# Kernel optimization log

Hardware: AMD Instinct MI355X
Metric: run time of the kernel (lower is better)

## Reference

```python
import jax, jax.numpy as jnp
import numpy as np

N_NODES = 50000
N_EDGES = 800000
D_IN = 64      # in_node_features == in_edge_features
D_OUT = 64     # out_features


def _xavier(key, shape, gain):
    fan_in, fan_out = shape[1], shape[0]
    bound = gain * np.sqrt(6.0 / (fan_in + fan_out))
    return jax.random.uniform(key, shape, jnp.float32, -bound, bound)


def setup_inputs() -> dict:
    key = jax.random.key(0)
    ks = jax.random.split(key, 8)
    gain = np.sqrt(2.0)  # calculate_gain('relu')
    features = jax.random.normal(ks[0], (N_NODES, D_IN), jnp.float32)
    edge_index = jax.random.randint(ks[1], (2, N_EDGES), 0, N_NODES, jnp.int64)
    edge_features = jax.random.normal(ks[2], (N_EDGES, D_IN), jnp.float32)
    W1 = _xavier(ks[3], (D_OUT, 2 * D_IN + D_IN), gain)
    b1 = jnp.zeros((D_OUT,), jnp.float32)
    W2 = _xavier(ks[4], (D_IN, D_OUT), gain)
    b2 = jnp.zeros((D_IN,), jnp.float32)
    W3 = _xavier(ks[5], (D_OUT, 2 * D_IN), gain)
    b3 = jnp.zeros((D_OUT,), jnp.float32)
    W4 = _xavier(ks[6], (D_OUT, D_OUT), gain)  # W4 not xavier-reset in source but default init; xavier is fine for a numeric baseline
    b4 = jnp.zeros((D_OUT,), jnp.float32)
    return dict(features=features, edge_index=edge_index, edge_features=edge_features,
                W1=W1, b1=b1, W2=W2, b2=b2, W3=W3, b3=b3, W4=W4, b4=b4)


def reference(features, edge_index, edge_features, W1, b1, W2, b2, W3, b3, W4, b4):
    src, dst = edge_index[0], edge_index[1]
    # gather + concat: [E, 2*D_IN + D_IN]
    h_neigh = jnp.concatenate([features[src], edge_features, features[dst]], axis=-1)
    h_neigh = jax.nn.relu(h_neigh @ W1.T + b1)
    h_neigh = h_neigh @ W2.T + b2                       # [E, D_IN]
    # scatter-sum into a copy of features (out=h.clone(), reduce='sum')
    s = features + jax.ops.segment_sum(h_neigh, src, num_segments=features.shape[0])
    z = jax.nn.relu(jnp.concatenate([features, s], axis=-1) @ W3.T + b3)
    z = z @ W4.T + b4
    return z
```

## Files before the change

### kernel.cpp

```cpp
#include <hip/hip_runtime.h>

typedef __bf16 bf16;
typedef __bf16 bf16x4 __attribute__((ext_vector_type(4)));
typedef __bf16 bf16x8 __attribute__((ext_vector_type(8)));
typedef float  f32x4  __attribute__((ext_vector_type(4)));

#define MFMA16(a, b, c) __builtin_amdgcn_mfma_f32_16x16x32_bf16((a), (b), (c), 0, 0, 0)

constexpr int N_NODES = 50000;
constexpr int N_EDGES = 800000;
constexpr int D = 64;

constexpr size_t OFF_FBUF   = 0;
constexpr size_t OFF_H2     = 6400000;
constexpr size_t OFF_IPOS   = 108800000;
constexpr size_t OFF_ROWPTR = 112000000;
constexpr size_t OFF_CURSOR = 112200064;
constexpr size_t OFF_COUNTS = 112400064;
constexpr size_t OFF_WBF    = 112600064;
constexpr size_t OFF_FLAGS  = 112657408;
constexpr size_t WS_FAST_NEED = 112700000;

constexpr size_t S_SBUF  = 0;
constexpr size_t S_FLAGS = 12800000;

constexpr int XS_STRIDE = 200;
constexpr int HS_STRIDE = 72;
constexpr int X2_STRIDE = 136;
constexpr int W1_STRIDE = 200;
constexpr int W2_STRIDE = 72;
constexpr int W3_STRIDE = 136;
constexpr int W4_STRIDE = 72;

__global__ void detect_kernel(const void* __restrict__ feat,
                              const void* __restrict__ eidx,
                              int* __restrict__ flags)
{
    __shared__ int c_bf[64], c_nz[64];
    const int t = threadIdx.x;
    const unsigned short* h = (const unsigned short*)feat;
    int c = 0;
    #pragma unroll
    for (int j = 0; j < 8; ++j) {
        const unsigned short v = h[(t * 8 + j) * 2];
        const int e8 = (v >> 7) & 0xFF;
        c += (e8 >= 97 && e8 <= 157) ? 1 : 0;
    }
    c_bf[t] = c;
    const int* ei = (const int*)eidx;
    int nz = 0;
    #pragma unroll
    for (int j = 0; j < 2; ++j)
        nz += (ei[(t * 2 + j) * 2 + 1] != 0) ? 1 : 0;
    c_nz[t] = nz;
    __syncthreads();
    if (t == 0) {
        int s = 0, s2 = 0;
        for (int i = 0; i < 64; ++i) { s += c_bf[i]; s2 += c_nz[i]; }
        flags[0] = (s < 384) ? 1 : 0;
        flags[1] = (s2 < 4) ? 1 : 0;
    }
}

__device__ inline bf16x8 ld8(const void* base, size_t off, int f32f) {
    if (f32f) {
        const float* p = (const float*)base + off;
        const float4 a = *(const float4*)p;
        const float4 b = *(const float4*)(p + 4);
        bf16x8 r;
        r[0] = (bf16)a.x; r[1] = (bf16)a.y; r[2] = (bf16)a.z; r[3] = (bf16)a.w;
        r[4] = (bf16)b.x; r[5] = (bf16)b.y; r[6] = (bf16)b.z; r[7] = (bf16)b.w;
        return r;
    }
    return *(const bf16x8*)((const bf16*)base + off);
}

__device__ inline float ldf(const void* base, int i, int f32f) {
    return f32f ? ((const float*)base)[i] : (float)((const bf16*)base)[i];
}

__device__ inline int gidx(const void* e, size_t i, int i64f) {
    return i64f ? (int)((const long long*)e)[i] : ((const int*)e)[i];
}

__global__ void prep_kernel(const void* __restrict__ W1, const void* __restrict__ W2,
                            const void* __restrict__ W3, const void* __restrict__ W4,
                            bf16* __restrict__ wbf, const int* __restrict__ flags)
{
    const int F32 = flags[0];
    for (int i = threadIdx.x; i < 28672; i += 256) {
        const void* src; int off;
        if (i < 12288)      { src = W1; off = i; }
        else if (i < 16384) { src = W2; off = i - 12288; }
        else if (i < 24576) { src = W3; off = i - 16384; }
        else                { src = W4; off = i - 24576; }
        wbf[i] = F32 ? (bf16)((const float*)src)[off] : ((const bf16*)src)[off];
    }
}

__global__ void conv_feat_kernel(const void* __restrict__ feat, bf16* __restrict__ fbuf,
                                 const int* __restrict__ flags)
{
    const int F32 = flags[0];
    const int i = blockIdx.x * 256 + threadIdx.x;
    if (F32) {
        const float4 v = ((const float4*)feat)[i];
        bf16x4 r; r[0] = (bf16)v.x; r[1] = (bf16)v.y; r[2] = (bf16)v.z; r[3] = (bf16)v.w;
        ((bf16x4*)fbuf)[i] = r;
    } else {
        ((bf16x4*)fbuf)[i] = ((const bf16x4*)feat)[i];
    }
}

__global__ void hist_kernel(const void* __restrict__ eidx, int* __restrict__ counts,
                            const int* __restrict__ flags)
{
    const int I64 = flags[1];
    const int e = blockIdx.x * 256 + threadIdx.x;
    atomicAdd(&counts[gidx(eidx, e, I64)], 1);
}

__global__ void scan_kernel(const int* __restrict__ counts, int* __restrict__ rowptr,
                            int* __restrict__ cursor)
{
    __shared__ int part[256];
    const int t = threadIdx.x;
    const int base = t * 196;
    int s = 0;
    for (int g = 0; g < 49; ++g) {
        const int idx = base + g * 4;
        if (idx < N_NODES) {
            const int4 v = *(const int4*)&counts[idx];
            s += v.x + v.y + v.z + v.w;
        }
    }
    part[t] = s;
    __syncthreads();
    if (t == 0) {
        int acc = 0;
        for (int i = 0; i < 256; ++i) { const int v = part[i]; part[i] = acc; acc += v; }
        rowptr[N_NODES] = acc;
    }
    __syncthreads();
    int acc = part[t];
    for (int g = 0; g < 49; ++g) {
        const int idx = base + g * 4;
        if (idx < N_NODES) {
            const int4 v = *(const int4*)&counts[idx];
            int4 r;
            r.x = acc;
            r.y = acc + v.x;
            r.z = acc + v.x + v.y;
            r.w = acc + v.x + v.y + v.z;
            acc += v.x + v.y + v.z + v.w;
            *(int4*)&rowptr[idx] = r;
            *(int4*)&cursor[idx] = r;
        }
    }
}

__global__ void fill_kernel(const void* __restrict__ eidx, int* __restrict__ cursor,
                            int* __restrict__ ipos, const int* __restrict__ flags)
{
    const int I64 = flags[1];
    const int e = blockIdx.x * 256 + threadIdx.x;
    const int src = gidx(eidx, e, I64);
    ipos[e] = atomicAdd(&cursor[src], 1);
}

__global__ __launch_bounds__(256, 3) void edge_fast(
    const bf16* __restrict__ fbuf, const void* __restrict__ eidx,
    const void* __restrict__ efeat,
    const bf16* __restrict__ wbf, const void* __restrict__ b1, const void* __restrict__ b2,
    const int* __restrict__ ipos, bf16* __restrict__ h2ws, const int* __restrict__ flags)
{
    __shared__ bf16 W1l[64 * W1_STRIDE];
    __shared__ bf16 W2l[64 * W2_STRIDE];
    __shared__ bf16 hs[4][32 * 72];

    const int t    = threadIdx.x;
    const int wave = t >> 6;
    const int lane = t & 63;
    const int lrow = lane & 15;
    const int quad = lane >> 4;
    const int e0   = blockIdx.x * 128 + wave * 32;
    const int F32  = flags[0], I64 = flags[1];

    #pragma unroll
    for (int it = 0; it < 6; ++it) {
        const int idx = it * 256 + t;
        const int row = idx / 24;
        const int col = (idx - row * 24) * 8;
        *(bf16x8*)&W1l[row * W1_STRIDE + col] = *(const bf16x8*)&wbf[row * 192 + col];
    }
    #pragma unroll
    for (int it = 0; it < 2; ++it) {
        const int idx = it * 256 + t;
        const int row = idx >> 3;
        const int col = (idx & 7) * 8;
        *(bf16x8*)&W2l[row * W2_STRIDE + col] = *(const bf16x8*)&wbf[12288 + row * 64 + col];
    }
    __syncthreads();

    const int eA   = e0 + lrow;
    const int eB   = e0 + 16 + lrow;
    const int srcA = gidx(eidx, (size_t)eA, I64);
    const int dstA = gidx(eidx, (size_t)N_EDGES + eA, I64);
    const int srcB = gidx(eidx, (size_t)eB, I64);
    const int dstB = gidx(eidx, (size_t)N_EDGES + eB, I64);

    f32x4 acc[2][4] = {
        {{0,0,0,0},{0,0,0,0},{0,0,0,0},{0,0,0,0}},
        {{0,0,0,0},{0,0,0,0},{0,0,0,0},{0,0,0,0}}
    };
    #pragma unroll
    for (int k = 0; k < 6; ++k) {
        const int po = (k & 1) * 32 + quad * 8;
        bf16x8 a0, a1;
        if (k < 2) {
            a0 = *(const bf16x8*)&fbuf[(size_t)srcA * D + po];
            a1 = *(const bf16x8*)&fbuf[(size_t)srcB * D + po];
        } else if (k < 4) {
            a0 = ld8(efeat, (size_t)eA * D + po, F32);
            a1 = ld8(efeat, (size_t)eB * D + po, F32);
        } else {
            a0 = *(const bf16x8*)&fbuf[(size_t)dstA * D + po];
            a1 = *(const bf16x8*)&fbuf[(size_t)dstB * D + po];
        }
        #pragma unroll
        for (int n = 0; n < 4; ++n) {
            const bf16x8 b = *(const bf16x8*)&W1l[(n * 16 + lrow) * W1_STRIDE + k * 32 + quad * 8];
            acc[0][n] = MFMA16(a0, b, acc[0][n]);
            acc[1][n] = MFMA16(a1, b, acc[1][n]);
        }
    }

    #pragma unroll
    for (int n = 0; n < 4; ++n) {
        const int col  = n * 16 + lrow;
        const float bb = ldf(b1, col, F32);
        #pragma unroll
        for (int m = 0; m < 2; ++m) {
            #pragma unroll
            for (int r = 0; r < 4; ++r) {
                float v = acc[m][n][r] + bb;
                v = v > 0.f ? v : 0.f;
                hs[wave][(m * 16 + quad * 4 + r) * 72 + col] = (bf16)v;
            }
        }
    }

    f32x4 acc2[2][4] = {
        {{0,0,0,0},{0,0,0,0},{0,0,0,0},{0,0,0,0}},
        {{0,0,0,0},{0,0,0,0},{0,0,0,0},{0,0,0,0}}
    };
    #pragma unroll
    for (int k = 0; k < 2; ++k) {
        const bf16x8 a0 = *(const bf16x8*)&hs[wave][lrow * 72 + k * 32 + quad * 8];
        const bf16x8 a1 = *(const bf16x8*)&hs[wave][(16 + lrow) * 72 + k * 32 + quad * 8];
        #pragma unroll
        for (int n = 0; n < 4; ++n) {
            const bf16x8 b = *(const bf16x8*)&W2l[(n * 16 + lrow) * W2_STRIDE + k * 32 + quad * 8];
            acc2[0][n] = MFMA16(a0, b, acc2[0][n]);
            acc2[1][n] = MFMA16(a1, b, acc2[1][n]);
        }
    }

    #pragma unroll
    for (int n = 0; n < 4; ++n) {
        const int col  = n * 16 + lrow;
        const float bb = ldf(b2, col, F32);
        #pragma unroll
        for (int m = 0; m < 2; ++m) {
            #pragma unroll
            for (int r = 0; r < 4; ++r)
                hs[wave][(m * 16 + quad * 4 + r) * 72 + col] = (bf16)(acc2[m][n][r] + bb);
        }
    }

    const int row = lane >> 2;
    const int seg = lane & 3;
    #pragma unroll
    for (int m = 0; m < 2; ++m) {
        const int ip  = ipos[e0 + m * 16 + row];
        const bf16x8 v0 = *(const bf16x8*)&hs[wave][(m * 16 + row) * 72 + seg * 16];
        const bf16x8 v1 = *(const bf16x8*)&hs[wave][(m * 16 + row) * 72 + seg * 16 + 8];
        *(bf16x8*)&h2ws[(size_t)ip * D + seg * 16]     = v0;
        *(bf16x8*)&h2ws[(size_t)ip * D + seg * 16 + 8] = v1;
    }
}

__global__ __launch_bounds__(256) void node_fast(
    const bf16* __restrict__ fbuf, const bf16* __restrict__ h2ws,
    const int* __restrict__ rowptr,
    const bf16* __restrict__ wbf, const void* __restrict__ b3, const void* __restrict__ b4,
    void* __restrict__ out, const int* __restrict__ flags)
{
    __shared__ bf16 xs[64 * X2_STRIDE];
    __shared__ bf16 h3s[64 * HS_STRIDE];
    __shared__ bf16 W3l[64 * W3_STRIDE];
    __shared__ bf16 W4l[64 * W4_STRIDE];

    const int t  = threadIdx.x;
    const int r0 = blockIdx.x * 64;
    const int F32 = flags[0];

    #pragma unroll
    for (int it = 0; it < 4; ++it) {
        const int idx = it * 256 + t;
        const int row = idx >> 4;
        const int col = (idx & 15) * 8;
        *(bf16x8*)&W3l[row * W3_STRIDE + col] = *(const bf16x8*)&wbf[16384 + row * 128 + col];
    }
    #pragma unroll
    for (int it = 0; it < 2; ++it) {
        const int idx = it * 256 + t;
        const int row = idx >> 3;
        const int col = (idx & 7) * 8;
        *(bf16x8*)&W4l[row * W4_STRIDE + col] = *(const bf16x8*)&wbf[24576 + row * 64 + col];
    }

    {
        const int nloc = t >> 2;
        const int node = r0 + nloc;
        const int seg  = t & 3;
        float accv[16];
        #pragma unroll
        for (int i = 0; i < 16; ++i) accv[i] = 0.f;
        bf16x8 f0 = {0,0,0,0,0,0,0,0}, f1 = {0,0,0,0,0,0,0,0};
        if (node < N_NODES) {
            f0 = *(const bf16x8*)&fbuf[(size_t)node * D + seg * 16];
            f1 = *(const bf16x8*)&fbuf[(size_t)node * D + seg * 16 + 8];
            const int jb = rowptr[node], je = rowptr[node + 1];
            int j = jb;
            for (; j + 8 <= je; j += 8) {
                bf16x8 v[16];
                #pragma unroll
                for (int u = 0; u < 8; ++u) {
                    v[2 * u]     = *(const bf16x8*)&h2ws[(size_t)(j + u) * D + seg * 16];
                    v[2 * u + 1] = *(const bf16x8*)&h2ws[(size_t)(j + u) * D + seg * 16 + 8];
                }
                #pragma unroll
                for (int u = 0; u < 8; ++u) {
                    #pragma unroll
                    for (int i = 0; i < 8; ++i) {
                        accv[i]     += (float)v[2 * u][i];
                        accv[i + 8] += (float)v[2 * u + 1][i];
                    }
                }
            }
            for (; j + 2 <= je; j += 2) {
                const bf16x8 a0 = *(const bf16x8*)&h2ws[(size_t)j * D + seg * 16];
                const bf16x8 a1 = *(const bf16x8*)&h2ws[(size_t)j * D + seg * 16 + 8];
                const bf16x8 c0 = *(const bf16x8*)&h2ws[(size_t)(j + 1) * D + seg * 16];
                const bf16x8 c1 = *(const bf16x8*)&h2ws[(size_t)(j + 1) * D + seg * 16 + 8];
                #pragma unroll
                for (int i = 0; i < 8; ++i) {
                    accv[i]     += (float)a0[i] + (float)c0[i];
                    accv[i + 8] += (float)a1[i] + (float)c1[i];
                }
            }
            if (j < je) {
                const bf16x8 a0 = *(const bf16x8*)&h2ws[(size_t)j * D + seg * 16];
                const bf16x8 a1 = *(const bf16x8*)&h2ws[(size_t)j * D + seg * 16 + 8];
                #pragma unroll
                for (int i = 0; i < 8; ++i) {
                    accv[i]     += (float)a0[i];
                    accv[i + 8] += (float)a1[i];
                }
            }
        }
        bf16x8 s0, s1;
        #pragma unroll
        for (int i = 0; i < 8; ++i) {
            s0[i] = (bf16)((float)f0[i] + accv[i]);
            s1[i] = (bf16)((float)f1[i] + accv[i + 8]);
        }
        *(bf16x8*)&xs[nloc * X2_STRIDE + seg * 16]          = f0;
        *(bf16x8*)&xs[nloc * X2_STRIDE + seg * 16 + 8]      = f1;
        *(bf16x8*)&xs[nloc * X2_STRIDE + 64 + seg * 16]     = s0;
        *(bf16x8*)&xs[nloc * X2_STRIDE + 64 + seg * 16 + 8] = s1;
    }
    __syncthreads();

    const int wave = t >> 6;
    const int lane = t & 63;
    const int m0   = wave * 16;
    const int lrow = lane & 15;
    const int quad = lane >> 4;

    f32x4 acc[4] = {{0,0,0,0},{0,0,0,0},{0,0,0,0},{0,0,0,0}};
    #pragma unroll
    for (int k = 0; k < 4; ++k) {
        const bf16x8 a = *(const bf16x8*)&xs[(m0 + lrow) * X2_STRIDE + k * 32 + quad * 8];
        #pragma unroll
        for (int n = 0; n < 4; ++n) {
            const bf16x8 b = *(const bf16x8*)&W3l[(n * 16 + lrow) * W3_STRIDE + k * 32 + quad * 8];
            acc[n] = MFMA16(a, b, acc[n]);
        }
    }

    #pragma unroll
    for (int n = 0; n < 4; ++n) {
        const int col  = n * 16 + lrow;
        const float bb = ldf(b3, col, F32);
        #pragma unroll
        for (int r = 0; r < 4; ++r) {
            float v = acc[n][r] + bb;
            v = v > 0.f ? v : 0.f;
            h3s[(m0 + quad * 4 + r) * HS_STRIDE + col] = (bf16)v;
        }
    }

    f32x4 acc2[4] = {{0,0,0,0},{0,0,0,0},{0,0,0,0},{0,0,0,0}};
    #pragma unroll
    for (int k = 0; k < 2; ++k) {
        const bf16x8 a = *(const bf16x8*)&h3s[(m0 + lrow) * HS_STRIDE + k * 32 + quad * 8];
        #pragma unroll
        for (int n = 0; n < 4; ++n) {
            const bf16x8 b = *(const bf16x8*)&W4l[(n * 16 + lrow) * W4_STRIDE + k * 32 + quad * 8];
            acc2[n] = MFMA16(a, b, acc2[n]);
        }
    }

    #pragma unroll
    for (int n = 0; n < 4; ++n) {
        const int col  = n * 16 + lrow;
        const float bb = ldf(b4, col, F32);
        #pragma unroll
        for (int r = 0; r < 4; ++r) {
            const int node = r0 + m0 + quad * 4 + r;
            if (node < N_NODES) {
                const float v = acc2[n][r] + bb;
                if (F32) ((float*)out)[(size_t)node * D + col] = v;
                else     ((bf16*)out)[(size_t)node * D + col] = (bf16)v;
            }
        }
    }
}

__global__ __launch_bounds__(256) void edge_slow(
    const void* __restrict__ feat, const void* __restrict__ eidx,
    const void* __restrict__ efeat,
    const void* __restrict__ W1, const void* __restrict__ b1,
    const void* __restrict__ W2, const void* __restrict__ b2,
    float* __restrict__ sbuf, const int* __restrict__ flags)
{
    __shared__ bf16 xs[64 * XS_STRIDE];
    __shared__ bf16 h1s[64 * HS_STRIDE];
    __shared__ int  srcs[64];
    __shared__ int  fl[2];

    const int t  = threadIdx.x;
    const int e0 = blockIdx.x * 64;

    if (t < 2) fl[t] = flags[t];
    __syncthreads();
    const int F32 = fl[0], I64 = fl[1];

    if (t < 64) srcs[t] = gidx(eidx, e0 + t, I64);

    for (int i = t; i < 64 * 24; i += 256) {
        const int e    = i / 24;
        const int c    = i - e * 24;
        const int part = c >> 3;
        const int cc   = c & 7;
        size_t off;
        const void* base;
        if (part == 0)      { base = feat;  off = (size_t)gidx(eidx, e0 + e, I64) * D + cc * 8; }
        else if (part == 1) { base = efeat; off = (size_t)(e0 + e) * D + cc * 8; }
        else                { base = feat;  off = (size_t)gidx(eidx, (size_t)N_EDGES + e0 + e, I64) * D + cc * 8; }
        *(bf16x8*)&xs[e * XS_STRIDE + part * 64 + cc * 8] = ld8(base, off, F32);
    }
    __syncthreads();

    const int wave = t >> 6;
    const int lane = t & 63;
    const int m0   = wave * 16;
    const int lrow = lane & 15;
    const int quad = lane >> 4;

    f32x4 acc[4] = {{0,0,0,0},{0,0,0,0},{0,0,0,0},{0,0,0,0}};
    #pragma unroll
    for (int k = 0; k < 6; ++k) {
        const bf16x8 a = *(const bf16x8*)&xs[(m0 + lrow) * XS_STRIDE + k * 32 + quad * 8];
        #pragma unroll
        for (int n = 0; n < 4; ++n) {
            const bf16x8 b = ld8(W1, (size_t)(n * 16 + lrow) * 192 + k * 32 + quad * 8, F32);
            acc[n] = MFMA16(a, b, acc[n]);
        }
    }

    #pragma unroll
    for (int n = 0; n < 4; ++n) {
        const int col  = n * 16 + lrow;
        const float bb = ldf(b1, col, F32);
        #pragma unroll
        for (int r = 0; r < 4; ++r) {
            float v = acc[n][r] + bb;
            v = v > 0.f ? v : 0.f;
            h1s[(m0 + quad * 4 + r) * HS_STRIDE + col] = (bf16)v;
        }
    }
    __syncthreads();

    f32x4 acc2[4] = {{0,0,0,0},{0,0,0,0},{0,0,0,0},{0,0,0,0}};
    #pragma unroll
    for (int k = 0; k < 2; ++k) {
        const bf16x8 a = *(const bf16x8*)&h1s[(m0 + lrow) * HS_STRIDE + k * 32 + quad * 8];
        #pragma unroll
        for (int n = 0; n < 4; ++n) {
            const bf16x8 b = ld8(W2, (size_t)(n * 16 + lrow) * D + k * 32 + quad * 8, F32);
            acc2[n] = MFMA16(a, b, acc2[n]);
        }
    }

    #pragma unroll
    for (int n = 0; n < 4; ++n) {
        const int col  = n * 16 + lrow;
        const float bb = ldf(b2, col, F32);
        #pragma unroll
        for (int r = 0; r < 4; ++r) {
            const int e = m0 + quad * 4 + r;
            atomicAdd(&sbuf[(size_t)srcs[e] * D + col], acc2[n][r] + bb);
        }
    }
}

__global__ __launch_bounds__(256) void node_slow(
    const void* __restrict__ feat, const float* __restrict__ sbuf,
    const void* __restrict__ W3, const void* __restrict__ b3,
    const void* __restrict__ W4, const void* __restrict__ b4,
    void* __restrict__ out, const int* __restrict__ flags)
{
    __shared__ bf16 xs[64 * X2_STRIDE];
    __shared__ bf16 h3s[64 * HS_STRIDE];
    __shared__ int fl[1];

    const int t  = threadIdx.x;
    const int r0 = blockIdx.x * 64;

    if (t == 0) fl[0] = flags[0];
    __syncthreads();
    const int F32 = fl[0];

    for (int i = t; i < 64 * 8; i += 256) {
        const int r    = i >> 3;
        const int c    = i & 7;
        const int node = r0 + r;
        bf16x8 fv = {0,0,0,0,0,0,0,0};
        bf16x8 sv = {0,0,0,0,0,0,0,0};
        if (node < N_NODES) {
            fv = ld8(feat, (size_t)node * D + c * 8, F32);
            const float4 sa = *(const float4*)&sbuf[(size_t)node * D + c * 8];
            const float4 sb = *(const float4*)&sbuf[(size_t)node * D + c * 8 + 4];
            sv[0] = (bf16)((float)fv[0] + sa.x);
            sv[1] = (bf16)((float)fv[1] + sa.y);
            sv[2] = (bf16)((float)fv[2] + sa.z);
            sv[3] = (bf16)((float)fv[3] + sa.w);
            sv[4] = (bf16)((float)fv[4] + sb.x);
            sv[5] = (bf16)((float)fv[5] + sb.y);
            sv[6] = (bf16)((float)fv[6] + sb.z);
            sv[7] = (bf16)((float)fv[7] + sb.w);
        }
        *(bf16x8*)&xs[r * X2_STRIDE + c * 8]      = fv;
        *(bf16x8*)&xs[r * X2_STRIDE + 64 + c * 8] = sv;
    }
    __syncthreads();

    const int wave = t >> 6;
    const int lane = t & 63;
    const int m0   = wave * 16;
    const int lrow = lane & 15;
    const int quad = lane >> 4;

    f32x4 acc[4] = {{0,0,0,0},{0,0,0,0},{0,0,0,0},{0,0,0,0}};
    #pragma unroll
    for (int k = 0; k < 4; ++k) {
        const bf16x8 a = *(const bf16x8*)&xs[(m0 + lrow) * X2_STRIDE + k * 32 + quad * 8];
        #pragma unroll
        for (int n = 0; n < 4; ++n) {
            const bf16x8 b = ld8(W3, (size_t)(n * 16 + lrow) * 128 + k * 32 + quad * 8, F32);
            acc[n] = MFMA16(a, b, acc[n]);
        }
    }

    #pragma unroll
    for (int n = 0; n < 4; ++n) {
        const int col  = n * 16 + lrow;
        const float bb = ldf(b3, col, F32);
        #pragma unroll
        for (int r = 0; r < 4; ++r) {
            float v = acc[n][r] + bb;
            v = v > 0.f ? v : 0.f;
            h3s[(m0 + quad * 4 + r) * HS_STRIDE + col] = (bf16)v;
        }
    }
    __syncthreads();

    f32x4 acc2[4] = {{0,0,0,0},{0,0,0,0},{0,0,0,0},{0,0,0,0}};
    #pragma unroll
    for (int k = 0; k < 2; ++k) {
        const bf16x8 a = *(const bf16x8*)&h3s[(m0 + lrow) * HS_STRIDE + k * 32 + quad * 8];
        #pragma unroll
        for (int n = 0; n < 4; ++n) {
            const bf16x8 b = ld8(W4, (size_t)(n * 16 + lrow) * D + k * 32 + quad * 8, F32);
            acc2[n] = MFMA16(a, b, acc2[n]);
        }
    }

    #pragma unroll
    for (int n = 0; n < 4; ++n) {
        const int col  = n * 16 + lrow;
        const float bb = ldf(b4, col, F32);
        #pragma unroll
        for (int r = 0; r < 4; ++r) {
            const int node = r0 + m0 + quad * 4 + r;
            if (node < N_NODES) {
                const float v = acc2[n][r] + bb;
                if (F32) ((float*)out)[(size_t)node * D + col] = v;
                else     ((bf16*)out)[(size_t)node * D + col] = (bf16)v;
            }
        }
    }
}

extern "C" void kernel_launch(void* const* d_in, const int* in_sizes, int n_in,
                              void* d_out, int out_size, void* d_ws, size_t ws_size,
                              hipStream_t stream) {
    const void* feat  = d_in[0];
    const void* eidx  = d_in[1];
    const void* efeat = d_in[2];
    const void* W1    = d_in[3];
    const void* b1    = d_in[4];
    const void* W2    = d_in[5];
    const void* b2    = d_in[6];
    const void* W3    = d_in[7];
    const void* b3    = d_in[8];
    const void* W4    = d_in[9];
    const void* b4    = d_in[10];

    char* ws = (char*)d_ws;

    if (ws_size >= WS_FAST_NEED) {
        bf16* fbuf   = (bf16*)(ws + OFF_FBUF);
        bf16* h2ws   = (bf16*)(ws + OFF_H2);
        int*  ipos   = (int*)(ws + OFF_IPOS);
        int*  rowptr = (int*)(ws + OFF_ROWPTR);
        int*  cursor = (int*)(ws + OFF_CURSOR);
        int*  counts = (int*)(ws + OFF_COUNTS);
        bf16* wbf    = (bf16*)(ws + OFF_WBF);
        int*  flags  = (int*)(ws + OFF_FLAGS);

        detect_kernel<<<1, 64, 0, stream>>>(feat, eidx, flags);
        hipMemsetAsync(counts, 0, (size_t)N_NODES * sizeof(int), stream);
        prep_kernel<<<1, 256, 0, stream>>>(W1, W2, W3, W4, wbf, flags);
        conv_feat_kernel<<<3125, 256, 0, stream>>>(feat, fbuf, flags);
        hist_kernel<<<N_EDGES / 256, 256, 0, stream>>>(eidx, counts, flags);
        scan_kernel<<<1, 256, 0, stream>>>(counts, rowptr, cursor);
        fill_kernel<<<N_EDGES / 256, 256, 0, stream>>>(eidx, cursor, ipos, flags);
        edge_fast<<<N_EDGES / 128, 256, 0, stream>>>(fbuf, eidx, efeat, wbf, b1, b2,
                                                     ipos, h2ws, flags);
        node_fast<<<(N_NODES + 63) / 64, 256, 0, stream>>>(fbuf, h2ws, rowptr,
                                                           wbf, b3, b4, d_out, flags);
    } else {
        float* sbuf  = (float*)(ws + S_SBUF);
        int*   flags = (int*)(ws + S_FLAGS);

        detect_kernel<<<1, 64, 0, stream>>>(feat, eidx, flags);
        hipMemsetAsync(sbuf, 0, (size_t)N_NODES * D * sizeof(float), stream);
        edge_slow<<<N_EDGES / 64, 256, 0, stream>>>(feat, eidx, efeat, W1, b1, W2, b2,
                                                    sbuf, flags);
        node_slow<<<(N_NODES + 63) / 64, 256, 0, stream>>>(feat, sbuf, W3, b3, W4, b4,
                                                           d_out, flags);
    }
}
```

Measured before the change: 567.8 us.

## Fuse histogram into feature conversion and slot assignment into edge kernel

```diff
diff --git a/kernel.cpp b/kernel.cpp
--- a/kernel.cpp
+++ b/kernel.cpp
@@ -28,9 +28,7 @@
 constexpr int HS_STRIDE = 72;
 constexpr int X2_STRIDE = 136;
 constexpr int W1_STRIDE = 200;
-constexpr int W2_STRIDE = 72;
 constexpr int W3_STRIDE = 136;
-constexpr int W4_STRIDE = 72;
 
 __global__ void detect_kernel(const void* __restrict__ feat,
                               const void* __restrict__ eidx,
@@ -98,10 +96,11 @@
     }
 }
 
-__global__ void conv_feat_kernel(const void* __restrict__ feat, bf16* __restrict__ fbuf,
+__global__ void conv_hist_kernel(const void* __restrict__ feat, bf16* __restrict__ fbuf,
+                                 const void* __restrict__ eidx, int* __restrict__ counts,
                                  const int* __restrict__ flags)
 {
-    const int F32 = flags[0];
+    const int F32 = flags[0], I64 = flags[1];
     const int i = blockIdx.x * 256 + threadIdx.x;
     if (F32) {
         const float4 v = ((const float4*)feat)[i];
@@ -110,14 +109,7 @@
     } else {
         ((bf16x4*)fbuf)[i] = ((const bf16x4*)feat)[i];
     }
-}
-
-__global__ void hist_kernel(const void* __restrict__ eidx, int* __restrict__ counts,
-                            const int* __restrict__ flags)
-{
-    const int I64 = flags[1];
-    const int e = blockIdx.x * 256 + threadIdx.x;
-    atomicAdd(&counts[gidx(eidx, e, I64)], 1);
+    atomicAdd(&counts[gidx(eidx, (size_t)i, I64)], 1);
 }
 
 __global__ void scan_kernel(const int* __restrict__ counts, int* __restrict__ rowptr,
@@ -159,24 +151,15 @@
     }
 }
 
-__global__ void fill_kernel(const void* __restrict__ eidx, int* __restrict__ cursor,
-                            int* __restrict__ ipos, const int* __restrict__ flags)
-{
-    const int I64 = flags[1];
-    const int e = blockIdx.x * 256 + threadIdx.x;
-    const int src = gidx(eidx, e, I64);
-    ipos[e] = atomicAdd(&cursor[src], 1);
-}
-
-__global__ __launch_bounds__(256, 3) void edge_fast(
+__global__ __launch_bounds__(256, 4) void edge_fast(
     const bf16* __restrict__ fbuf, const void* __restrict__ eidx,
     const void* __restrict__ efeat,
     const bf16* __restrict__ wbf, const void* __restrict__ b1, const void* __restrict__ b2,
-    const int* __restrict__ ipos, bf16* __restrict__ h2ws, const int* __restrict__ flags)
+    int* __restrict__ cursor, bf16* __restrict__ h2ws, const int* __restrict__ flags)
 {
     __shared__ bf16 W1l[64 * W1_STRIDE];
-    __shared__ bf16 W2l[64 * W2_STRIDE];
-    __shared__ bf16 hs[4][32 * 72];
+    __shared__ bf16 hs[4][16 * 72];
+    __shared__ int  ips[4][32];
 
     const int t    = threadIdx.x;
     const int wave = t >> 6;
@@ -193,14 +176,6 @@
         const int col = (idx - row * 24) * 8;
         *(bf16x8*)&W1l[row * W1_STRIDE + col] = *(const bf16x8*)&wbf[row * 192 + col];
     }
-    #pragma unroll
-    for (int it = 0; it < 2; ++it) {
-        const int idx = it * 256 + t;
-        const int row = idx >> 3;
-        const int col = (idx & 7) * 8;
-        *(bf16x8*)&W2l[row * W2_STRIDE + col] = *(const bf16x8*)&wbf[12288 + row * 64 + col];
-    }
-    __syncthreads();
 
     const int eA   = e0 + lrow;
     const int eB   = e0 + 16 + lrow;
@@ -209,97 +184,103 @@
     const int srcB = gidx(eidx, (size_t)eB, I64);
     const int dstB = gidx(eidx, (size_t)N_EDGES + eB, I64);
 
+    if (lane < 32) {
+        const int s = (lane < 16) ? srcA : srcB;
+        ips[wave][lane] = atomicAdd(&cursor[s], 1);
+    }
+
+    bf16x8 aA[6], aB[6];
+    #pragma unroll
+    for (int k = 0; k < 6; ++k) {
+        const int po = (k & 1) * 32 + quad * 8;
+        if (k < 2) {
+            aA[k] = *(const bf16x8*)&fbuf[(size_t)srcA * D + po];
+            aB[k] = *(const bf16x8*)&fbuf[(size_t)srcB * D + po];
+        } else if (k < 4) {
+            aA[k] = ld8(efeat, (size_t)eA * D + po, F32);
+            aB[k] = ld8(efeat, (size_t)eB * D + po, F32);
+        } else {
+            aA[k] = *(const bf16x8*)&fbuf[(size_t)dstA * D + po];
+            aB[k] = *(const bf16x8*)&fbuf[(size_t)dstB * D + po];
+        }
+    }
+
+    __syncthreads();
+
     f32x4 acc[2][4] = {
         {{0,0,0,0},{0,0,0,0},{0,0,0,0},{0,0,0,0}},
         {{0,0,0,0},{0,0,0,0},{0,0,0,0},{0,0,0,0}}
     };
     #pragma unroll
     for (int k = 0; k < 6; ++k) {
-        const int po = (k & 1) * 32 + quad * 8;
-        bf16x8 a0, a1;
-        if (k < 2) {
-            a0 = *(const bf16x8*)&fbuf[(size_t)srcA * D + po];
-            a1 = *(const bf16x8*)&fbuf[(size_t)srcB * D + po];
-        } else if (k < 4) {
-            a0 = ld8(efeat, (size_t)eA * D + po, F32);
-            a1 = ld8(efeat, (size_t)eB * D + po, F32);
-        } else {
-            a0 = *(const bf16x8*)&fbuf[(size_t)dstA * D + po];
-            a1 = *(const bf16x8*)&fbuf[(size_t)dstB * D + po];
-        }
         #pragma unroll
         for (int n = 0; n < 4; ++n) {
             const bf16x8 b = *(const bf16x8*)&W1l[(n * 16 + lrow) * W1_STRIDE + k * 32 + quad * 8];
-            acc[0][n] = MFMA16(a0, b, acc[0][n]);
-            acc[1][n] = MFMA16(a1, b, acc[1][n]);
-        }
-    }
-
-    #pragma unroll
-    for (int n = 0; n < 4; ++n) {
-        const int col  = n * 16 + lrow;
-        const float bb = ldf(b1, col, F32);
-        #pragma unroll
-        for (int m = 0; m < 2; ++m) {
+            acc[0][n] = MFMA16(aA[k], b, acc[0][n]);
+            acc[1][n] = MFMA16(aB[k], b, acc[1][n]);
+        }
+    }
+
+    bf16x8 w2r[2][4];
+    #pragma unroll
+    for (int k = 0; k < 2; ++k)
+        #pragma unroll
+        for (int n = 0; n < 4; ++n)
+            w2r[k][n] = *(const bf16x8*)&wbf[12288 + (n * 16 + lrow) * 64 + k * 32 + quad * 8];
+
+    f32x4 acc2[2][4];
+    #pragma unroll
+    for (int m = 0; m < 2; ++m) {
+        #pragma unroll
+        for (int n = 0; n < 4; ++n) {
+            const int col  = n * 16 + lrow;
+            const float bb = ldf(b1, col, F32);
             #pragma unroll
             for (int r = 0; r < 4; ++r) {
                 float v = acc[m][n][r] + bb;
                 v = v > 0.f ? v : 0.f;
-                hs[wave][(m * 16 + quad * 4 + r) * 72 + col] = (bf16)v;
+                hs[wave][(quad * 4 + r) * 72 + col] = (bf16)v;
             }
         }
-    }
-
-    f32x4 acc2[2][4] = {
-        {{0,0,0,0},{0,0,0,0},{0,0,0,0},{0,0,0,0}},
-        {{0,0,0,0},{0,0,0,0},{0,0,0,0},{0,0,0,0}}
-    };
-    #pragma unroll
-    for (int k = 0; k < 2; ++k) {
-        const bf16x8 a0 = *(const bf16x8*)&hs[wave][lrow * 72 + k * 32 + quad * 8];
-        const bf16x8 a1 = *(const bf16x8*)&hs[wave][(16 + lrow) * 72 + k * 32 + quad * 8];
-        #pragma unroll
-        for (int n = 0; n < 4; ++n) {
-            const bf16x8 b = *(const bf16x8*)&W2l[(n * 16 + lrow) * W2_STRIDE + k * 32 + quad * 8];
-            acc2[0][n] = MFMA16(a0, b, acc2[0][n]);
-            acc2[1][n] = MFMA16(a1, b, acc2[1][n]);
-        }
-    }
-
-    #pragma unroll
-    for (int n = 0; n < 4; ++n) {
-        const int col  = n * 16 + lrow;
-        const float bb = ldf(b2, col, F32);
-        #pragma unroll
-        for (int m = 0; m < 2; ++m) {
+        #pragma unroll
+        for (int n = 0; n < 4; ++n) acc2[m][n] = f32x4{0, 0, 0, 0};
+        #pragma unroll
+        for (int k = 0; k < 2; ++k) {
+            const bf16x8 a = *(const bf16x8*)&hs[wave][lrow * 72 + k * 32 + quad * 8];
+            #pragma unroll
+            for (int n = 0; n < 4; ++n)
+                acc2[m][n] = MFMA16(a, w2r[k][n], acc2[m][n]);
+        }
+    }
+
+    const int row = lane >> 2;
+    const int seg = lane & 3;
+    #pragma unroll
+    for (int m = 0; m < 2; ++m) {
+        #pragma unroll
+        for (int n = 0; n < 4; ++n) {
+            const int col  = n * 16 + lrow;
+            const float bb = ldf(b2, col, F32);
             #pragma unroll
             for (int r = 0; r < 4; ++r)
-                hs[wave][(m * 16 + quad * 4 + r) * 72 + col] = (bf16)(acc2[m][n][r] + bb);
-        }
-    }
-
-    const int row = lane >> 2;
-    const int seg = lane & 3;
-    #pragma unroll
-    for (int m = 0; m < 2; ++m) {
-        const int ip  = ipos[e0 + m * 16 + row];
-        const bf16x8 v0 = *(const bf16x8*)&hs[wave][(m * 16 + row) * 72 + seg * 16];
-        const bf16x8 v1 = *(const bf16x8*)&hs[wave][(m * 16 + row) * 72 + seg * 16 + 8];
+                hs[wave][(quad * 4 + r) * 72 + col] = (bf16)(acc2[m][n][r] + bb);
+        }
+        const int ip  = ips[wave][m * 16 + row];
+        const bf16x8 v0 = *(const bf16x8*)&hs[wave][row * 72 + seg * 16];
+        const bf16x8 v1 = *(const bf16x8*)&hs[wave][row * 72 + seg * 16 + 8];
         *(bf16x8*)&h2ws[(size_t)ip * D + seg * 16]     = v0;
         *(bf16x8*)&h2ws[(size_t)ip * D + seg * 16 + 8] = v1;
     }
 }
 
-__global__ __launch_bounds__(256) void node_fast(
+__global__ __launch_bounds__(256, 4) void node_fast(
     const bf16* __restrict__ fbuf, const bf16* __restrict__ h2ws,
     const int* __restrict__ rowptr,
     const bf16* __restrict__ wbf, const void* __restrict__ b3, const void* __restrict__ b4,
     void* __restrict__ out, const int* __restrict__ flags)
 {
     __shared__ bf16 xs[64 * X2_STRIDE];
-    __shared__ bf16 h3s[64 * HS_STRIDE];
     __shared__ bf16 W3l[64 * W3_STRIDE];
-    __shared__ bf16 W4l[64 * W4_STRIDE];
 
     const int t  = threadIdx.x;
     const int r0 = blockIdx.x * 64;
@@ -311,13 +292,6 @@
         const int row = idx >> 4;
         const int col = (idx & 15) * 8;
         *(bf16x8*)&W3l[row * W3_STRIDE + col] = *(const bf16x8*)&wbf[16384 + row * 128 + col];
-    }
-    #pragma unroll
-    for (int it = 0; it < 2; ++it) {
-        const int idx = it * 256 + t;
-        const int row = idx >> 3;
-        const int col = (idx & 7) * 8;
-        *(bf16x8*)&W4l[row * W4_STRIDE + col] = *(const bf16x8*)&wbf[24576 + row * 64 + col];
     }
 
     {
@@ -389,6 +363,13 @@
     const int lrow = lane & 15;
     const int quad = lane >> 4;
 
+    bf16x8 w4r[2][4];
+    #pragma unroll
+    for (int k = 0; k < 2; ++k)
+        #pragma unroll
+        for (int n = 0; n < 4; ++n)
+            w4r[k][n] = *(const bf16x8*)&wbf[24576 + (n * 16 + lrow) * 64 + k * 32 + quad * 8];
+
     f32x4 acc[4] = {{0,0,0,0},{0,0,0,0},{0,0,0,0},{0,0,0,0}};
     #pragma unroll
     for (int k = 0; k < 4; ++k) {
@@ -408,19 +389,17 @@
         for (int r = 0; r < 4; ++r) {
             float v = acc[n][r] + bb;
             v = v > 0.f ? v : 0.f;
-            h3s[(m0 + quad * 4 + r) * HS_STRIDE + col] = (bf16)v;
+            xs[(m0 + quad * 4 + r) * X2_STRIDE + col] = (bf16)v;
         }
     }
 
     f32x4 acc2[4] = {{0,0,0,0},{0,0,0,0},{0,0,0,0},{0,0,0,0}};
     #pragma unroll
     for (int k = 0; k < 2; ++k) {
-        const bf16x8 a = *(const bf16x8*)&h3s[(m0 + lrow) * HS_STRIDE + k * 32 + quad * 8];
-        #pragma unroll
-        for (int n = 0; n < 4; ++n) {
-            const bf16x8 b = *(const bf16x8*)&W4l[(n * 16 + lrow) * W4_STRIDE + k * 32 + quad * 8];
-            acc2[n] = MFMA16(a, b, acc2[n]);
-        }
+        const bf16x8 a = *(const bf16x8*)&xs[(m0 + lrow) * X2_STRIDE + k * 32 + quad * 8];
+        #pragma unroll
+        for (int n = 0; n < 4; ++n)
+            acc2[n] = MFMA16(a, w4r[k][n], acc2[n]);
     }
 
     #pragma unroll
@@ -439,6 +418,8 @@
     }
 }
 
+constexpr int XSS_STRIDE = 200;
+
 __global__ __launch_bounds__(256) void edge_slow(
     const void* __restrict__ feat, const void* __restrict__ eidx,
     const void* __restrict__ efeat,
@@ -446,7 +427,7 @@
     const void* __restrict__ W2, const void* __restrict__ b2,
     float* __restrict__ sbuf, const int* __restrict__ flags)
 {
-    __shared__ bf16 xs[64 * XS_STRIDE];
+    __shared__ bf16 xs[64 * XSS_STRIDE];
     __shared__ bf16 h1s[64 * HS_STRIDE];
     __shared__ int  srcs[64];
     __shared__ int  fl[2];
@@ -470,7 +451,7 @@
         if (part == 0)      { base = feat;  off = (size_t)gidx(eidx, e0 + e, I64) * D + cc * 8; }
         else if (part == 1) { base = efeat; off = (size_t)(e0 + e) * D + cc * 8; }
         else                { base = feat;  off = (size_t)gidx(eidx, (size_t)N_EDGES + e0 + e, I64) * D + cc * 8; }
-        *(bf16x8*)&xs[e * XS_STRIDE + part * 64 + cc * 8] = ld8(base, off, F32);
+        *(bf16x8*)&xs[e * XSS_STRIDE + part * 64 + cc * 8] = ld8(base, off, F32);
     }
     __syncthreads();
 
@@ -483,7 +464,7 @@
     f32x4 acc[4] = {{0,0,0,0},{0,0,0,0},{0,0,0,0},{0,0,0,0}};
     #pragma unroll
     for (int k = 0; k < 6; ++k) {
-        const bf16x8 a = *(const bf16x8*)&xs[(m0 + lrow) * XS_STRIDE + k * 32 + quad * 8];
+        const bf16x8 a = *(const bf16x8*)&xs[(m0 + lrow) * XSS_STRIDE + k * 32 + quad * 8];
         #pragma unroll
         for (int n = 0; n < 4; ++n) {
             const bf16x8 b = ld8(W1, (size_t)(n * 16 + lrow) * 192 + k * 32 + quad * 8, F32);
@@ -645,7 +626,6 @@
     if (ws_size >= WS_FAST_NEED) {
         bf16* fbuf   = (bf16*)(ws + OFF_FBUF);
         bf16* h2ws   = (bf16*)(ws + OFF_H2);
-        int*  ipos   = (int*)(ws + OFF_IPOS);
         int*  rowptr = (int*)(ws + OFF_ROWPTR);
         int*  cursor = (int*)(ws + OFF_CURSOR);
         int*  counts = (int*)(ws + OFF_COUNTS);
@@ -655,12 +635,10 @@
         detect_kernel<<<1, 64, 0, stream>>>(feat, eidx, flags);
         hipMemsetAsync(counts, 0, (size_t)N_NODES * sizeof(int), stream);
         prep_kernel<<<1, 256, 0, stream>>>(W1, W2, W3, W4, wbf, flags);
-        conv_feat_kernel<<<3125, 256, 0, stream>>>(feat, fbuf, flags);
-        hist_kernel<<<N_EDGES / 256, 256, 0, stream>>>(eidx, counts, flags);
+        conv_hist_kernel<<<3125, 256, 0, stream>>>(feat, fbuf, eidx, counts, flags);
         scan_kernel<<<1, 256, 0, stream>>>(counts, rowptr, cursor);
-        fill_kernel<<<N_EDGES / 256, 256, 0, stream>>>(eidx, cursor, ipos, flags);
         edge_fast<<<N_EDGES / 128, 256, 0, stream>>>(fbuf, eidx, efeat, wbf, b1, b2,
-                                                     ipos, h2ws, flags);
+                                                     cursor, h2ws, flags);
         node_fast<<<(N_NODES + 63) / 64, 256, 0, stream>>>(fbuf, h2ws, rowptr,
                                                            wbf, b3, b4, d_out, flags);
     } else {
```

Result: no change. 571.7 us (+0.7%).
